# Kernel tuning notes

Hardware: AMD Instinct MI355X
Metric: run time of the kernel (lower is better)

## Reference

```python
import jax, jax.numpy as jnp
import numpy as np

N_AGENTS = 10
N_ENEMIES = 11
N_ALLIES = 9
H = 64           # rnn_hidden_dim
HYP = 64         # api_hyper_dim
DEPTH = 2        # residual_depth
OWN = 32
EF = 10          # enemy_feats_dim
AF = 10          # ally_feats_dim
N_ACTIONS = 17
BS = 1024


def _hypernet(x, win, bin_, wres, bres, wout, bout):
    # Linear -> ReLU -> DEPTH x (ReLU(Linear)+identity) -> Linear
    h = jax.nn.relu(x @ win + bin_)
    for d in range(DEPTH):
        h = jax.nn.relu(h @ wres[d] + bres[d]) + h
    return h @ wout + bout


def _gru_cell(x, h, wi, wh, bi, bh):
    gi = x @ wi + bi
    gh = h @ wh + bh
    ir, iz, in_ = jnp.split(gi, 3, axis=-1)
    hr, hz, hn = jnp.split(gh, 3, axis=-1)
    r = jax.nn.sigmoid(ir + hr)
    z = jax.nn.sigmoid(iz + hz)
    n = jnp.tanh(in_ + r * hn)
    return (1.0 - z) * n + z * h


def setup_inputs() -> dict:
    key = jax.random.key(0)
    ks = iter(jax.random.split(key, 48))
    def p(shape, s=0.1):
        return jax.random.normal(next(ks), shape, jnp.float32) * s
    N = BS * N_AGENTS
    inp = {
        'own_feats':    p((N, OWN), 1.0),
        'enemy_feats':  p((N * N_ENEMIES, EF), 1.0),
        'ally_feats':   p((N * N_ALLIES, AF), 1.0),
        'hidden_state': p((N, H), 1.0),
        'fc1_w': p((OWN, H)), 'fc1_b': p((H,)),
        'agent_emb': p((N_AGENTS, H)), 'action_emb': p((N_ACTIONS, H)),
        'hen_win': p((EF, HYP)), 'hen_bin': p((HYP,)),
        'hen_wres': p((DEPTH, HYP, HYP)), 'hen_bres': p((DEPTH, HYP)),
        'hen_wout': p((HYP, EF * H)), 'hen_bout': p((EF * H,)),
        'hal_win': p((AF, HYP)), 'hal_bin': p((HYP,)),
        'hal_wres': p((DEPTH, HYP, HYP)), 'hal_bres': p((DEPTH, HYP)),
        'hal_wout': p((HYP, AF * H)), 'hal_bout': p((AF * H,)),
        'gru_wi': p((H, 3 * H)), 'gru_wh': p((H, 3 * H)),
        'gru_bi': p((3 * H,)), 'gru_bh': p((3 * H,)),
        'fc2_w': p((H, 6)), 'fc2_b': p((6,)),
        'how_win': p((EF, HYP)), 'how_bin': p((HYP,)),
        'how_wres': p((DEPTH, HYP, HYP)), 'how_bres': p((DEPTH, HYP)),
        'how_wout': p((HYP, H)), 'how_bout': p((H,)),
        'hob_win': p((EF, HYP)), 'hob_bin': p((HYP,)),
        'hob_wres': p((DEPTH, HYP, HYP)), 'hob_bres': p((DEPTH, HYP)),
        'hob_wout': p((HYP, 1)), 'hob_bout': p((1,)),
        'agent_idx': jax.random.randint(next(ks), (N,), 0, N_AGENTS),
        'last_action_idx': jax.random.randint(next(ks), (N,), 0, N_ACTIONS),
        'bs': BS,
    }
    return inp


def reference(own_feats, enemy_feats, ally_feats, hidden_state,
              fc1_w, fc1_b, agent_emb, action_emb,
              hen_win, hen_bin, hen_wres, hen_bres, hen_wout, hen_bout,
              hal_win, hal_bin, hal_wres, hal_bres, hal_wout, hal_bout,
              gru_wi, gru_wh, gru_bi, gru_bh,
              fc2_w, fc2_b,
              how_win, how_bin, how_wres, how_bres, how_wout, how_bout,
              hob_win, hob_bin, hob_wres, hob_bres, hob_wout, hob_bout,
              agent_idx, last_action_idx, bs):
    N = bs * N_AGENTS
    # own embedding + id embeddings
    emb = own_feats @ fc1_w + fc1_b
    emb = emb + agent_emb[agent_idx] + action_emb[last_action_idx]
    # per-enemy hypernet weights [N*NE, EF, H]; bmm + sum-pool over enemies
    w_en = _hypernet(enemy_feats, hen_win, hen_bin, hen_wres, hen_bres,
                     hen_wout, hen_bout).reshape(-1, EF, H)
    emb_en = jnp.einsum('nf,nfh->nh', enemy_feats, w_en)
    emb_en = emb_en.reshape(N, N_ENEMIES, H).sum(axis=1)
    # per-ally hypernet weights + bmm + sum-pool
    w_al = _hypernet(ally_feats, hal_win, hal_bin, hal_wres, hal_bres,
                     hal_wout, hal_bout).reshape(-1, AF, H)
    emb_al = jnp.einsum('nf,nfh->nh', ally_feats, w_al)
    emb_al = emb_al.reshape(N, N_ALLIES, H).sum(axis=1)
    x = jax.nn.relu(emb + emb_en + emb_al)
    hh = _gru_cell(x, hidden_state.reshape(-1, H), gru_wi, gru_wh, gru_bi, gru_bh)
    q_normal = (hh @ fc2_w + fc2_b).reshape(bs, N_AGENTS, 6)
    # attack-action head: hypernet-generated per-enemy weights/biases
    ow = _hypernet(enemy_feats, how_win, how_bin, how_wres, how_bres,
                   how_wout, how_bout).reshape(N, N_ENEMIES, H)
    ob = _hypernet(enemy_feats, hob_win, hob_bin, hob_wres, hob_bres,
                   hob_wout, hob_bout).reshape(N, N_ENEMIES)
    q_attack = (jnp.einsum('nh,neh->ne', hh, ow) + ob).reshape(bs, N_AGENTS, N_ENEMIES)
    q = jnp.concatenate([q_normal, q_attack], axis=-1)
    return q, hh.reshape(bs, N_AGENTS, H)
```

## Files before the change

### kernel.cpp

```cpp
#include <hip/hip_runtime.h>

#define DI static __device__ __forceinline__

typedef short s16x8 __attribute__((ext_vector_type(8)));
typedef float f32x4 __attribute__((ext_vector_type(4)));
typedef float f32x2 __attribute__((ext_vector_type(2)));
typedef unsigned u32x2 __attribute__((ext_vector_type(2)));

DI unsigned short f2b(float f) {
  union { float f; unsigned u; } v; v.f = f;
  return (unsigned short)((v.u + 0x7FFF + ((v.u >> 16) & 1)) >> 16);
}
DI float b2f(unsigned short s) {
  union { unsigned u; float f; } v; v.u = ((unsigned)s) << 16;
  return v.f;
}
DI unsigned cvtpk(float lo, float hi) {
  unsigned r;
  asm("v_cvt_pk_bf16_f32 %0, %1, %2" : "=v"(r) : "v"(lo), "v"(hi));
  return r;
}
DI f32x4 MFMA(s16x8 a, s16x8 b, f32x4 c) {
  return __builtin_amdgcn_mfma_f32_16x16x32_bf16(a, b, c, 0, 0, 0);
}
DI s16x8 ldg8(const unsigned short* p) { return *(const s16x8*)p; }

#define OFF_WEN   0
#define OFF_WAL   10240
#define OFF_WHOW  20480
#define OFF_WHOB  30720
#define OFF_BGEN  40960
#define OFF_BGAL  83968
#define OFF_WIT   126976
#define OFF_WHT   139264
#define OFF_FC1T  151552
#define OFF_FC2E  153600
#define OFF_HOWT  154624
#define OFF_HOBT  158720
#define SH_END    159744
#define B_EMB_EN  (SH_END*2)
#define B_EMB_AL  (B_EMB_EN + 2621440)
#define B_HB      (B_EMB_AL + 2621440)
#define B_GBF     (B_HB + 40960)

#define XSTR 40
#define HSTR 72
#define PSTR 680

__global__ __launch_bounds__(256) void kprep(
    const float* __restrict__ hen_win, const float* __restrict__ hen_wres,
    const float* __restrict__ hal_win, const float* __restrict__ hal_wres,
    const float* __restrict__ how_win, const float* __restrict__ how_wres,
    const float* __restrict__ hob_win, const float* __restrict__ hob_wres,
    const float* __restrict__ hen_wout, const float* __restrict__ hen_bout,
    const float* __restrict__ hal_wout, const float* __restrict__ hal_bout,
    const float* __restrict__ gru_wi, const float* __restrict__ gru_wh,
    const float* __restrict__ fc1_w, const float* __restrict__ fc2_w,
    const float* __restrict__ how_bout, const float* __restrict__ how_wout,
    const float* __restrict__ hob_wout,
    unsigned short* __restrict__ ws)
{
  const int gid = blockIdx.x * 256 + threadIdx.x;
  const int gsz = gridDim.x * 256;
  for (int i = gid; i < 4 * 10240; i += gsz) {
    int s = i / 10240, idx = i - s * 10240;
    const float* win  = (s == 0) ? hen_win  : (s == 1) ? hal_win  : (s == 2) ? how_win  : hob_win;
    const float* wres = (s == 0) ? hen_wres : (s == 1) ? hal_wres : (s == 2) ? how_wres : hob_wres;
    float v;
    if (idx < 2048) { int n = idx >> 5, k = idx & 31; v = (k < 10) ? win[k*64 + n] : 0.f; }
    else { int r = idx - 2048; int d = r >> 12; int r2 = r & 4095; int n = r2 >> 6, k = r2 & 63;
           v = wres[d*4096 + k*64 + n]; }
    ws[s * 10240 + idx] = f2b(v);
  }
  for (int i = gid; i < 2 * 43008; i += gsz) {
    int s = i / 43008, idx = i - s * 43008;
    const float* wout = s ? hal_wout : hen_wout;
    const float* bout = s ? hal_bout : hen_bout;
    int kl = idx & 31, n = (idx >> 5) & 63, c = idx >> 11;
    int kfg = c * 32 + kl;
    float v = 0.f;
    if (kfg < 640)      { int k = kfg / 10, f = kfg - k * 10; v = wout[k*640 + f*64 + n]; }
    else if (kfg < 650) { v = bout[(kfg - 640)*64 + n]; }
    ws[(s ? OFF_BGAL : OFF_BGEN) + idx] = f2b(v);
  }
  for (int i = gid; i < 2 * 12288; i += gsz) {
    int s = i / 12288, idx = i - s * 12288;
    int n = idx >> 6, k = idx & 63;
    const float* w = s ? gru_wh : gru_wi;
    ws[(s ? OFF_WHT : OFF_WIT) + idx] = f2b(w[k*192 + n]);
  }
  for (int i = gid; i < 2048; i += gsz) { int n = i >> 5, k = i & 31; ws[OFF_FC1T + i] = f2b(fc1_w[k*64 + n]); }
  for (int i = gid; i < 1024; i += gsz) {
    int n = i >> 6, k = i & 63;
    float v = 0.f; if (n < 6) v = fc2_w[k*6 + n]; else if (n == 6) v = how_bout[k];
    ws[OFF_FC2E + i] = f2b(v);
  }
  for (int i = gid; i < 4096; i += gsz) ws[OFF_HOWT + i] = f2b(how_wout[i]);
}

template<int TMAX, bool WLAST>
DI void stack_batch(const unsigned short* __restrict__ x_lds,
                    unsigned short* const (&hbp)[TMAX], const int (&tis)[TMAX], int E,
                    const unsigned short* __restrict__ wg,
                    const float* __restrict__ bin, const float* __restrict__ bres,
                    f32x4 (&hval)[TMAX][4])
{
  const int l = threadIdx.x & 63;
  const int lrow = l & 15, gq = l >> 4, lk8 = gq * 8;
  {
    s16x8 wf[4]; f32x4 bv[4];
#pragma unroll
    for (int mt = 0; mt < 4; mt++) {
      wf[mt] = ldg8(wg + (mt*16 + lrow)*32 + lk8);
      bv[mt] = *(const f32x4*)(bin + mt*16 + gq*4);
    }
#pragma unroll
    for (int tt = 0; tt < TMAX; tt++) {
      if (tis[tt] < E) {
        s16x8 xf = *(const s16x8*)&x_lds[(tis[tt]*16 + lrow)*XSTR + lk8];
#pragma unroll
        for (int mt = 0; mt < 4; mt++) {
          f32x4 d = MFMA(wf[mt], xf, f32x4{0.f,0.f,0.f,0.f});
#pragma unroll
          for (int r = 0; r < 4; r++) hval[tt][mt][r] = fmaxf(d[r] + bv[mt][r], 0.f);
        }
        unsigned short* wr = hbp[tt] + lrow*HSTR;
#pragma unroll
        for (int mt = 0; mt < 4; mt++) {
          u32x2 pw;
          pw.x = cvtpk(hval[tt][mt][0], hval[tt][mt][1]);
          pw.y = cvtpk(hval[tt][mt][2], hval[tt][mt][3]);
          *(u32x2*)&wr[mt*16 + gq*4] = pw;
        }
      }
    }
  }
#pragma unroll
  for (int d = 0; d < 2; d++) {
    const unsigned short* wt = wg + 2048 + d * 4096;
    s16x8 wf[4][2]; f32x4 bv[4];
#pragma unroll
    for (int mt = 0; mt < 4; mt++) {
      wf[mt][0] = ldg8(wt + (mt*16 + lrow)*64 + lk8);
      wf[mt][1] = ldg8(wt + (mt*16 + lrow)*64 + 32 + lk8);
      bv[mt] = *(const f32x4*)(bres + d*64 + mt*16 + gq*4);
    }
#pragma unroll
    for (int tt = 0; tt < TMAX; tt++) {
      if (tis[tt] < E) {
        const unsigned short* hr = hbp[tt] + lrow*HSTR;
        s16x8 b0 = *(const s16x8*)&hr[lk8];
        s16x8 b1 = *(const s16x8*)&hr[32 + lk8];
#pragma unroll
        for (int mt = 0; mt < 4; mt++) {
          f32x4 a = MFMA(wf[mt][0], b0, f32x4{0.f,0.f,0.f,0.f});
          a = MFMA(wf[mt][1], b1, a);
#pragma unroll
          for (int r = 0; r < 4; r++)
            hval[tt][mt][r] = fmaxf(a[r] + bv[mt][r], 0.f) + hval[tt][mt][r];
        }
        if (d == 0 || WLAST) {
          unsigned short* wr = hbp[tt] + lrow*HSTR;
#pragma unroll
          for (int mt = 0; mt < 4; mt++) {
            u32x2 pw;
            pw.x = cvtpk(hval[tt][mt][0], hval[tt][mt][1]);
            pw.y = cvtpk(hval[tt][mt][2], hval[tt][mt][3]);
            *(u32x2*)&wr[mt*16 + gq*4] = pw;
          }
        }
      }
    }
  }
}

template<int E>
DI void hyp_body16(const float* __restrict__ feats,
                   const unsigned short* __restrict__ Wg, const unsigned short* __restrict__ Bg,
                   const float* __restrict__ bin, const float* __restrict__ bres,
                   float* __restrict__ emb, char* smem)
{
  unsigned short* x_lds = (unsigned short*)smem;
  unsigned short* h_lds = (unsigned short*)(smem + 14080);
  unsigned short* P     = (unsigned short*)smem;
  const int t = threadIdx.x;
  const int l = t & 63, wv = t >> 6;
  const int lrow = l & 15, gq = l >> 4, lk8 = gq * 8, lr4 = gq * 4;

  for (int idx = t; idx < E * 512; idx += 256) {
    int row = idx >> 5, c = idx & 31;
    x_lds[row*XSTR + c] = (c < 10) ? f2b(feats[row*10 + c]) : (unsigned short)0;
  }
  __syncthreads();

  int tis[3] = {wv, wv + 4, wv + 8};
  unsigned short* hbp[3] = { h_lds + (wv)*16*HSTR, h_lds + (wv+4)*16*HSTR, h_lds + (wv+8)*16*HSTR };
  f32x4 hval[3][4];
  stack_batch<3, true>(x_lds, hbp, tis, E, Wg, bin, bres, hval);
  __syncthreads();

  const int a = t >> 4, kq = t & 15, k0 = kq * 4;
  float acc[4][10];
#pragma unroll
  for (int kk = 0; kk < 4; kk++)
#pragma unroll
    for (int f = 0; f < 10; f++) acc[kk][f] = 0.f;
#pragma unroll
  for (int e = 0; e < E; e++) {
    int row = a * E + e;
    const unsigned short* xr = x_lds + row * XSTR;
    s16x8 xv8 = *(const s16x8*)xr;
    unsigned xv2 = *(const unsigned*)(xr + 8);
    float xf[10];
#pragma unroll
    for (int f = 0; f < 8; f++) xf[f] = b2f((unsigned short)xv8[f]);
    xf[8] = b2f((unsigned short)(xv2 & 0xFFFF));
    xf[9] = b2f((unsigned short)(xv2 >> 16));
    u32x2 hp = *(const u32x2*)&h_lds[row*HSTR + k0];
    float hf[4] = { b2f((unsigned short)(hp.x & 0xFFFF)), b2f((unsigned short)(hp.x >> 16)),
                    b2f((unsigned short)(hp.y & 0xFFFF)), b2f((unsigned short)(hp.y >> 16)) };
#pragma unroll
    for (int kk = 0; kk < 4; kk++)
#pragma unroll
      for (int f = 0; f < 10; f++) acc[kk][f] += hf[kk] * xf[f];
  }
  float sxv = 0.f; int a2 = 0, fx = 0;
  if (t < 160) {
    a2 = t / 10; fx = t - a2 * 10;
    for (int e = 0; e < E; e++) sxv += feats[(a2*E + e)*10 + fx];
  }
  __syncthreads();

  u32x2* Pw = (u32x2*)(P + a*PSTR + k0*10);
#pragma unroll
  for (int m = 0; m < 10; m++) {
    const int s0 = 4*m, s1 = 4*m+1, s2 = 4*m+2, s3 = 4*m+3;
    u32x2 pw;
    pw.x = cvtpk(acc[s0/10][s0%10], acc[s1/10][s1%10]);
    pw.y = cvtpk(acc[s2/10][s2%10], acc[s3/10][s3%10]);
    Pw[m] = pw;
  }
  if (t < 160) P[a2*PSTR + 640 + fx] = f2b(sxv);
  for (int i = t; i < 352; i += 256) { int a3 = i / 22, c = i - a3*22; P[a3*PSTR + 650 + c] = 0; }
  __syncthreads();

  f32x4 acc0 = {0.f,0.f,0.f,0.f}, acc1 = {0.f,0.f,0.f,0.f};
  const unsigned short* Bw = Bg + (wv*16 + lrow)*32 + lk8;
#pragma unroll
  for (int c = 0; c < 21; c++) {
    s16x8 af = *(const s16x8*)&P[lrow*PSTR + c*32 + lk8];
    s16x8 bf = ldg8(Bw + c*2048);
    if (c & 1) acc1 = MFMA(af, bf, acc1); else acc0 = MFMA(af, bf, acc0);
  }
#pragma unroll
  for (int r = 0; r < 4; r++)
    emb[(lr4 + r)*64 + wv*16 + lrow] = acc0[r] + acc1[r];
}

__global__ __launch_bounds__(256) void khyp_ea(
    const float* __restrict__ en_feats, const float* __restrict__ al_feats,
    const unsigned short* __restrict__ ws,
    const float* __restrict__ en_bin, const float* __restrict__ en_bres,
    const float* __restrict__ al_bin, const float* __restrict__ al_bres,
    float* __restrict__ emb_en, float* __restrict__ emb_al)
{
  __shared__ __align__(16) char smem[39424];
  if (blockIdx.x < 640) {
    int blk = blockIdx.x;
    hyp_body16<11>(en_feats + (long)blk*1760, ws + OFF_WEN, ws + OFF_BGEN,
                   en_bin, en_bres, emb_en + (long)blk*1024, smem);
  } else {
    int blk = blockIdx.x - 640;
    hyp_body16<9>(al_feats + (long)blk*1440, ws + OFF_WAL, ws + OFF_BGAL,
                  al_bin, al_bres, emb_al + (long)blk*1024, smem);
  }
}

__global__ __launch_bounds__(256) void kfused(
    const float* __restrict__ own, const float* __restrict__ agent_emb,
    const float* __restrict__ action_emb,
    const int* __restrict__ agent_idx, const int* __restrict__ last_action,
    const float* __restrict__ emb_en, const float* __restrict__ emb_al,
    const float* __restrict__ hidden,
    const unsigned short* __restrict__ ws,
    const float* __restrict__ fc1_b, const float* __restrict__ bi,
    const float* __restrict__ bh, const float* __restrict__ fc2_b,
    float* __restrict__ qout, float* __restrict__ hhout,
    unsigned short* __restrict__ g_bf, float* __restrict__ hb)
{
  __shared__ unsigned short own_lds[16*32];
  __shared__ unsigned short x_lds[16*HSTR];
  __shared__ unsigned short hp_lds[16*HSTR];
  __shared__ unsigned short hh_lds[16*HSTR];
  const int t = threadIdx.x;
  const int l = t & 63, wv = t >> 6;
  const int lrow = l & 15, lk8 = (l >> 4) * 8, lr4 = (l >> 4) * 4;
  const int n0 = blockIdx.x * 16;

  const unsigned short* fc1T = ws + OFF_FC1T;
  const unsigned short* wiT  = ws + OFF_WIT;
  const unsigned short* whT  = ws + OFF_WHT;
  const unsigned short* howT = ws + OFF_HOWT;
  const unsigned short* fc2e = ws + OFF_FC2E;

  for (int i = t; i < 512; i += 256) own_lds[i] = f2b(own[n0*32 + i]);
  for (int i = t; i < 1024; i += 256) hp_lds[(i >> 6)*HSTR + (i & 63)] = f2b(hidden[n0*64 + i]);
  __syncthreads();

  const int j = wv * 16 + lrow;
  {
    s16x8 a0 = *(const s16x8*)&own_lds[lrow*32 + lk8];
    s16x8 b0 = ldg8(fc1T + (wv*16 + lrow)*32 + lk8);
    f32x4 c0 = MFMA(a0, b0, f32x4{0.f,0.f,0.f,0.f});
    float fb = fc1_b[j];
#pragma unroll
    for (int r = 0; r < 4; r++) {
      int aa = lr4 + r; int n = n0 + aa;
      int ai = agent_idx[n], la = last_action[n];
      float v = c0[r] + fb + agent_emb[ai*64 + j] + action_emb[la*64 + j]
              + emb_en[n*64 + j] + emb_al[n*64 + j];
      x_lds[aa*HSTR + j] = f2b(fmaxf(v, 0.f));
    }
  }
  __syncthreads();

  {
    s16x8 xa[2], ha[2];
#pragma unroll
    for (int s = 0; s < 2; s++) {
      xa[s] = *(const s16x8*)&x_lds[lrow*HSTR + s*32 + lk8];
      ha[s] = *(const s16x8*)&hp_lds[lrow*HSTR + s*32 + lk8];
    }
    f32x4 gi[3], gh[3];
#pragma unroll
    for (int g3 = 0; g3 < 3; g3++) { gi[g3] = f32x4{0.f,0.f,0.f,0.f}; gh[g3] = f32x4{0.f,0.f,0.f,0.f}; }
#pragma unroll
    for (int g3 = 0; g3 < 3; g3++) {
      int tl = wv + g3 * 4;
#pragma unroll
      for (int s = 0; s < 2; s++) {
        gi[g3] = MFMA(xa[s], ldg8(wiT + (tl*16 + lrow)*64 + s*32 + lk8), gi[g3]);
        gh[g3] = MFMA(ha[s], ldg8(whT + (tl*16 + lrow)*64 + s*32 + lk8), gh[g3]);
      }
    }
    float bir = bi[j], biz = bi[64 + j], bin_ = bi[128 + j];
    float bhr = bh[j], bhz = bh[64 + j], bhn = bh[128 + j];
#pragma unroll
    for (int r = 0; r < 4; r++) {
      int aa = lr4 + r; int n = n0 + aa;
      float rr = 1.f / (1.f + __expf(-(gi[0][r] + bir + gh[0][r] + bhr)));
      float zz = 1.f / (1.f + __expf(-(gi[1][r] + biz + gh[1][r] + bhz)));
      float nn = tanhf(gi[2][r] + bin_ + rr * (gh[2][r] + bhn));
      float hp = hidden[n*64 + j];
      float hhv = (1.f - zz) * nn + zz * hp;
      hhout[n*64 + j] = hhv;
      hh_lds[aa*HSTR + j] = f2b(hhv);
    }
  }
  __syncthreads();

  {
    s16x8 hha[2];
#pragma unroll
    for (int s = 0; s < 2; s++) hha[s] = *(const s16x8*)&hh_lds[lrow*HSTR + s*32 + lk8];
    f32x4 gc = {0.f,0.f,0.f,0.f};
#pragma unroll
    for (int s = 0; s < 2; s++) gc = MFMA(hha[s], ldg8(howT + (wv*16 + lrow)*64 + s*32 + lk8), gc);
#pragma unroll
    for (int r = 0; r < 4; r++) g_bf[(n0 + lr4 + r)*64 + wv*16 + lrow] = f2b(gc[r]);
    if (wv == 0) {
      f32x4 qc = {0.f,0.f,0.f,0.f};
#pragma unroll
      for (int s = 0; s < 2; s++) qc = MFMA(hha[s], ldg8(fc2e + lrow*64 + s*32 + lk8), qc);
#pragma unroll
      for (int r = 0; r < 4; r++) {
        int n = n0 + lr4 + r;
        if (lrow < 6)       qout[n*17 + lrow] = qc[r] + fc2_b[lrow];
        else if (lrow == 6) hb[n] = qc[r];
      }
    }
  }
}

__global__ __launch_bounds__(256) void kattack(
    const float* __restrict__ en_feats, const unsigned short* __restrict__ ws,
    const float* __restrict__ how_bin, const float* __restrict__ how_bres,
    const float* __restrict__ hob_bin, const float* __restrict__ hob_bres,
    const unsigned short* __restrict__ g_bf, const float* __restrict__ hbuf,
    const float* __restrict__ hob_wout, const float* __restrict__ hob_bout,
    float* __restrict__ qout)
{
  __shared__ __align__(16) char smem[41728];
  unsigned short* x_lds = (unsigned short*)smem;
  unsigned short* scr   = (unsigned short*)(smem + 14080);
  const int t = threadIdx.x;
  const int l = t & 63, wv = t >> 6;
  const int lrow = l & 15, gq = l >> 4;
  const int blk = blockIdx.x;
  const float* feats = en_feats + (long)blk * 1760;

  for (int idx = t; idx < 176*32; idx += 256) {
    int row = idx >> 5, c = idx & 31;
    x_lds[row*XSTR + c] = (c < 10) ? f2b(feats[row*10 + c]) : (unsigned short)0;
  }
  __syncthreads();

  int tis[3] = {wv, wv + 4, wv + 8};
  unsigned short* hbp[3] = { scr + (wv*3+0)*16*HSTR, scr + (wv*3+1)*16*HSTR, scr + (wv*3+2)*16*HSTR };
  f32x4 hval[3][4];

  stack_batch<3, false>(x_lds, hbp, tis, 11, ws + OFF_WHOB, hob_bin, hob_bres, hval);
  f32x4 hw[4];
#pragma unroll
  for (int mt = 0; mt < 4; mt++) hw[mt] = *(const f32x4*)(hob_wout + mt*16 + gq*4);
  float qbv[3] = {0.f, 0.f, 0.f};
#pragma unroll
  for (int tt = 0; tt < 3; tt++) {
    if (tis[tt] < 11) {
      float s = 0.f;
#pragma unroll
      for (int mt = 0; mt < 4; mt++)
#pragma unroll
        for (int r = 0; r < 4; r++) s += hval[tt][mt][r] * hw[mt][r];
      s += __shfl_xor(s, 16, 64);
      s += __shfl_xor(s, 32, 64);
      qbv[tt] = s;
    }
  }

  stack_batch<3, false>(x_lds, hbp, tis, 11, ws + OFF_WHOW, how_bin, how_bres, hval);
  const float hob_b0 = hob_bout[0];
#pragma unroll
  for (int tt = 0; tt < 3; tt++) {
    if (tis[tt] < 11) {
      int row = tis[tt]*16 + lrow;
      int ag = (unsigned)row / 11u;
      int n = blk*16 + ag;
      float s = 0.f;
#pragma unroll
      for (int mt = 0; mt < 4; mt++) {
        u32x2 gv = *(const u32x2*)(g_bf + (long)n*64 + mt*16 + gq*4);
        s += hval[tt][mt][0] * b2f((unsigned short)(gv.x & 0xFFFF))
           + hval[tt][mt][1] * b2f((unsigned short)(gv.x >> 16))
           + hval[tt][mt][2] * b2f((unsigned short)(gv.y & 0xFFFF))
           + hval[tt][mt][3] * b2f((unsigned short)(gv.y >> 16));
      }
      s += __shfl_xor(s, 16, 64);
      s += __shfl_xor(s, 32, 64);
      if (l < 16) {
        int e = row - ag * 11;
        qout[n*17 + 6 + e] = s + qbv[tt] + hbuf[n] + hob_b0;
      }
    }
  }
}

extern "C" void kernel_launch(void* const* d_in, const int* in_sizes, int n_in,
                              void* d_out, int out_size, void* d_ws, size_t ws_size,
                              hipStream_t stream)
{
  (void)in_sizes; (void)n_in; (void)out_size; (void)ws_size;
  const float* own        = (const float*)d_in[0];
  const float* enemy      = (const float*)d_in[1];
  const float* ally       = (const float*)d_in[2];
  const float* hidden     = (const float*)d_in[3];
  const float* fc1_w      = (const float*)d_in[4];
  const float* fc1_b      = (const float*)d_in[5];
  const float* agent_emb  = (const float*)d_in[6];
  const float* action_emb = (const float*)d_in[7];
  const float* hen_win  = (const float*)d_in[8];  const float* hen_bin  = (const float*)d_in[9];
  const float* hen_wres = (const float*)d_in[10]; const float* hen_bres = (const float*)d_in[11];
  const float* hen_wout = (const float*)d_in[12]; const float* hen_bout = (const float*)d_in[13];
  const float* hal_win  = (const float*)d_in[14]; const float* hal_bin  = (const float*)d_in[15];
  const float* hal_wres = (const float*)d_in[16]; const float* hal_bres = (const float*)d_in[17];
  const float* hal_wout = (const float*)d_in[18]; const float* hal_bout = (const float*)d_in[19];
  const float* gru_wi = (const float*)d_in[20];   const float* gru_wh = (const float*)d_in[21];
  const float* gru_bi = (const float*)d_in[22];   const float* gru_bh = (const float*)d_in[23];
  const float* fc2_w  = (const float*)d_in[24];   const float* fc2_b  = (const float*)d_in[25];
  const float* how_win  = (const float*)d_in[26]; const float* how_bin  = (const float*)d_in[27];
  const float* how_wres = (const float*)d_in[28]; const float* how_bres = (const float*)d_in[29];
  const float* how_wout = (const float*)d_in[30]; const float* how_bout = (const float*)d_in[31];
  const float* hob_win  = (const float*)d_in[32]; const float* hob_bin  = (const float*)d_in[33];
  const float* hob_wres = (const float*)d_in[34]; const float* hob_bres = (const float*)d_in[35];
  const float* hob_wout = (const float*)d_in[36]; const float* hob_bout = (const float*)d_in[37];
  const int* agent_idx   = (const int*)d_in[38];
  const int* last_action = (const int*)d_in[39];

  unsigned short* ws = (unsigned short*)d_ws;
  float* emb_en = (float*)((char*)d_ws + B_EMB_EN);
  float* emb_al = (float*)((char*)d_ws + B_EMB_AL);
  float* hb     = (float*)((char*)d_ws + B_HB);
  unsigned short* g_bf = (unsigned short*)((char*)d_ws + B_GBF);

  float* q  = (float*)d_out;
  float* hh = q + 1024*10*17;

  kprep<<<128, 256, 0, stream>>>(hen_win, hen_wres, hal_win, hal_wres,
      how_win, how_wres, hob_win, hob_wres,
      hen_wout, hen_bout, hal_wout, hal_bout,
      gru_wi, gru_wh, fc1_w, fc2_w, how_bout, how_wout, hob_wout, ws);
  khyp_ea<<<1280, 256, 0, stream>>>(enemy, ally, ws,
      hen_bin, hen_bres, hal_bin, hal_bres, emb_en, emb_al);
  kfused<<<640, 256, 0, stream>>>(own, agent_emb, action_emb, agent_idx, last_action,
      emb_en, emb_al, hidden, ws, fc1_b, gru_bi, gru_bh, fc2_b, q, hh, g_bf, hb);
  kattack<<<640, 256, 0, stream>>>(enemy, ws, how_bin, how_bres, hob_bin, hob_bres,
      g_bf, hb, hob_wout, hob_bout, q);
}
```

Measured before the change: 78.49 us.

## Restructure hypernet kernels to one agent per 16-row tile with padded entity planes

The hypernet tiles change from packing 11 or 9 entities contiguously into 16-row MFMA tiles to giving each agent its own 16-row tile, zero-padded to 16 entities, with a compact plane layout in LDS. The per-agent outer product x^T h is now computed with an MFMA instead of scalar FMAs, and blocks handle 8 agents instead of 16, so khyp_ea and kattack launch twice as many blocks with about half the shared memory each. This removes the divergent tile-bound checks and the scalar pooling loop, and should raise occupancy. The cost is wasted MFMA work on padding rows (5/16 or 7/16 of each tile) and more blocks overall.

Result: slower. 106.0 us (+35.0%).

```diff
diff --git a/kernel.cpp b/kernel.cpp
--- a/kernel.cpp
+++ b/kernel.cpp
@@ -4,7 +4,6 @@
 
 typedef short s16x8 __attribute__((ext_vector_type(8)));
 typedef float f32x4 __attribute__((ext_vector_type(4)));
-typedef float f32x2 __attribute__((ext_vector_type(2)));
 typedef unsigned u32x2 __attribute__((ext_vector_type(2)));
 
 DI unsigned short f2b(float f) {
@@ -36,16 +35,14 @@
 #define OFF_FC1T  151552
 #define OFF_FC2E  153600
 #define OFF_HOWT  154624
-#define OFF_HOBT  158720
 #define SH_END    159744
 #define B_EMB_EN  (SH_END*2)
 #define B_EMB_AL  (B_EMB_EN + 2621440)
 #define B_HB      (B_EMB_AL + 2621440)
 #define B_GBF     (B_HB + 40960)
 
-#define XSTR 40
+#define PSTR 680
 #define HSTR 72
-#define PSTR 680
 
 __global__ __launch_bounds__(256) void kprep(
     const float* __restrict__ hen_win, const float* __restrict__ hen_wres,
@@ -57,7 +54,6 @@
     const float* __restrict__ gru_wi, const float* __restrict__ gru_wh,
     const float* __restrict__ fc1_w, const float* __restrict__ fc2_w,
     const float* __restrict__ how_bout, const float* __restrict__ how_wout,
-    const float* __restrict__ hob_wout,
     unsigned short* __restrict__ ws)
 {
   const int gid = blockIdx.x * 256 + threadIdx.x;
@@ -98,14 +94,13 @@
   for (int i = gid; i < 4096; i += gsz) ws[OFF_HOWT + i] = f2b(how_wout[i]);
 }
 
-template<int TMAX, bool WLAST>
-DI void stack_batch(const unsigned short* __restrict__ x_lds,
-                    unsigned short* const (&hbp)[TMAX], const int (&tis)[TMAX], int E,
-                    const unsigned short* __restrict__ wg,
-                    const float* __restrict__ bin, const float* __restrict__ bres,
-                    f32x4 (&hval)[TMAX][4])
-{
-  const int l = threadIdx.x & 63;
+DI void stack_planes(const unsigned short* __restrict__ x_lds,
+                     unsigned short* __restrict__ h2,
+                     const unsigned short* __restrict__ wg,
+                     const float* __restrict__ bin, const float* __restrict__ bres,
+                     f32x4 (&hval)[2][4])
+{
+  const int l = threadIdx.x & 63, wv = threadIdx.x >> 6;
   const int lrow = l & 15, gq = l >> 4, lk8 = gq * 8;
   {
     s16x8 wf[4]; f32x4 bv[4];
@@ -115,146 +110,146 @@
       bv[mt] = *(const f32x4*)(bin + mt*16 + gq*4);
     }
 #pragma unroll
-    for (int tt = 0; tt < TMAX; tt++) {
-      if (tis[tt] < E) {
-        s16x8 xf = *(const s16x8*)&x_lds[(tis[tt]*16 + lrow)*XSTR + lk8];
-#pragma unroll
-        for (int mt = 0; mt < 4; mt++) {
-          f32x4 d = MFMA(wf[mt], xf, f32x4{0.f,0.f,0.f,0.f});
-#pragma unroll
-          for (int r = 0; r < 4; r++) hval[tt][mt][r] = fmaxf(d[r] + bv[mt][r], 0.f);
-        }
-        unsigned short* wr = hbp[tt] + lrow*HSTR;
-#pragma unroll
-        for (int mt = 0; mt < 4; mt++) {
-          u32x2 pw;
-          pw.x = cvtpk(hval[tt][mt][0], hval[tt][mt][1]);
-          pw.y = cvtpk(hval[tt][mt][2], hval[tt][mt][3]);
-          *(u32x2*)&wr[mt*16 + gq*4] = pw;
-        }
+    for (int tt = 0; tt < 2; tt++) {
+      int a = wv + tt*4;
+      s16x8 xf = *(const s16x8*)&x_lds[(a*16 + lrow)*16 + lk8];
+      unsigned short* hw = h2 + a*1024 + lrow*16 + gq*4;
+#pragma unroll
+      for (int mt = 0; mt < 4; mt++) {
+        f32x4 d = MFMA(wf[mt], xf, f32x4{0.f,0.f,0.f,0.f});
+#pragma unroll
+        for (int r = 0; r < 4; r++) hval[tt][mt][r] = fmaxf(d[r] + bv[mt][r], 0.f);
+        u32x2 pw; pw.x = cvtpk(hval[tt][mt][0], hval[tt][mt][1]);
+        pw.y = cvtpk(hval[tt][mt][2], hval[tt][mt][3]);
+        *(u32x2*)(hw + mt*256) = pw;
       }
     }
   }
 #pragma unroll
   for (int d = 0; d < 2; d++) {
     const unsigned short* wt = wg + 2048 + d * 4096;
-    s16x8 wf[4][2]; f32x4 bv[4];
+    s16x8 wf0[4], wf1[4]; f32x4 bv[4];
 #pragma unroll
     for (int mt = 0; mt < 4; mt++) {
-      wf[mt][0] = ldg8(wt + (mt*16 + lrow)*64 + lk8);
-      wf[mt][1] = ldg8(wt + (mt*16 + lrow)*64 + 32 + lk8);
+      wf0[mt] = ldg8(wt + (mt*16 + lrow)*64 + lk8);
+      wf1[mt] = ldg8(wt + (mt*16 + lrow)*64 + 32 + lk8);
       bv[mt] = *(const f32x4*)(bres + d*64 + mt*16 + gq*4);
     }
 #pragma unroll
-    for (int tt = 0; tt < TMAX; tt++) {
-      if (tis[tt] < E) {
-        const unsigned short* hr = hbp[tt] + lrow*HSTR;
-        s16x8 b0 = *(const s16x8*)&hr[lk8];
-        s16x8 b1 = *(const s16x8*)&hr[32 + lk8];
-#pragma unroll
-        for (int mt = 0; mt < 4; mt++) {
-          f32x4 a = MFMA(wf[mt][0], b0, f32x4{0.f,0.f,0.f,0.f});
-          a = MFMA(wf[mt][1], b1, a);
-#pragma unroll
-          for (int r = 0; r < 4; r++)
-            hval[tt][mt][r] = fmaxf(a[r] + bv[mt][r], 0.f) + hval[tt][mt][r];
-        }
-        if (d == 0 || WLAST) {
-          unsigned short* wr = hbp[tt] + lrow*HSTR;
-#pragma unroll
-          for (int mt = 0; mt < 4; mt++) {
-            u32x2 pw;
-            pw.x = cvtpk(hval[tt][mt][0], hval[tt][mt][1]);
-            pw.y = cvtpk(hval[tt][mt][2], hval[tt][mt][3]);
-            *(u32x2*)&wr[mt*16 + gq*4] = pw;
-          }
-        }
-      }
-    }
+    for (int tt = 0; tt < 2; tt++) {
+      int a = wv + tt*4;
+      const unsigned short* hr = h2 + a*1024;
+      s16x8 b0 = *(const s16x8*)&hr[(gq>>1)*256 + lrow*16 + (gq&1)*8];
+      s16x8 b1 = *(const s16x8*)&hr[(2 + (gq>>1))*256 + lrow*16 + (gq&1)*8];
+      unsigned short* hw = h2 + a*1024 + lrow*16 + gq*4;
+#pragma unroll
+      for (int mt = 0; mt < 4; mt++) {
+        f32x4 acc = MFMA(wf0[mt], b0, f32x4{0.f,0.f,0.f,0.f});
+        acc = MFMA(wf1[mt], b1, acc);
+#pragma unroll
+        for (int r = 0; r < 4; r++)
+          hval[tt][mt][r] = fmaxf(acc[r] + bv[mt][r], 0.f) + hval[tt][mt][r];
+        u32x2 pw; pw.x = cvtpk(hval[tt][mt][0], hval[tt][mt][1]);
+        pw.y = cvtpk(hval[tt][mt][2], hval[tt][mt][3]);
+        *(u32x2*)(hw + mt*256) = pw;
+      }
+    }
+  }
+}
+
+DI void stage_x(const float* __restrict__ feats, int E, unsigned short* x_lds) {
+  for (int idx = threadIdx.x; idx < 136*16; idx += 256) {
+    int row = idx >> 4, c = idx & 15;
+    int a = row >> 4, e = row & 15;
+    float v = (a < 8 && e < E && c < 10) ? feats[(a*E + e)*10 + c] : 0.f;
+    x_lds[idx] = f2b(v);
   }
 }
 
 template<int E>
-DI void hyp_body16(const float* __restrict__ feats,
-                   const unsigned short* __restrict__ Wg, const unsigned short* __restrict__ Bg,
-                   const float* __restrict__ bin, const float* __restrict__ bres,
-                   float* __restrict__ emb, char* smem)
+DI void hyp_body(const float* __restrict__ feats,
+                 const unsigned short* __restrict__ Wg, const unsigned short* __restrict__ Bg,
+                 const float* __restrict__ bin, const float* __restrict__ bres,
+                 float* __restrict__ emb, char* smem)
 {
   unsigned short* x_lds = (unsigned short*)smem;
-  unsigned short* h_lds = (unsigned short*)(smem + 14080);
-  unsigned short* P     = (unsigned short*)smem;
+  unsigned short* h2    = (unsigned short*)(smem + 4352);
+  unsigned short* P2    = (unsigned short*)smem;
   const int t = threadIdx.x;
   const int l = t & 63, wv = t >> 6;
-  const int lrow = l & 15, gq = l >> 4, lk8 = gq * 8, lr4 = gq * 4;
-
-  for (int idx = t; idx < E * 512; idx += 256) {
-    int row = idx >> 5, c = idx & 31;
-    x_lds[row*XSTR + c] = (c < 10) ? f2b(feats[row*10 + c]) : (unsigned short)0;
-  }
-  __syncthreads();
-
-  int tis[3] = {wv, wv + 4, wv + 8};
-  unsigned short* hbp[3] = { h_lds + (wv)*16*HSTR, h_lds + (wv+4)*16*HSTR, h_lds + (wv+8)*16*HSTR };
-  f32x4 hval[3][4];
-  stack_batch<3, true>(x_lds, hbp, tis, E, Wg, bin, bres, hval);
-  __syncthreads();
-
-  const int a = t >> 4, kq = t & 15, k0 = kq * 4;
-  float acc[4][10];
-#pragma unroll
-  for (int kk = 0; kk < 4; kk++)
-#pragma unroll
-    for (int f = 0; f < 10; f++) acc[kk][f] = 0.f;
-#pragma unroll
-  for (int e = 0; e < E; e++) {
-    int row = a * E + e;
-    const unsigned short* xr = x_lds + row * XSTR;
-    s16x8 xv8 = *(const s16x8*)xr;
-    unsigned xv2 = *(const unsigned*)(xr + 8);
-    float xf[10];
-#pragma unroll
-    for (int f = 0; f < 8; f++) xf[f] = b2f((unsigned short)xv8[f]);
-    xf[8] = b2f((unsigned short)(xv2 & 0xFFFF));
-    xf[9] = b2f((unsigned short)(xv2 >> 16));
-    u32x2 hp = *(const u32x2*)&h_lds[row*HSTR + k0];
-    float hf[4] = { b2f((unsigned short)(hp.x & 0xFFFF)), b2f((unsigned short)(hp.x >> 16)),
-                    b2f((unsigned short)(hp.y & 0xFFFF)), b2f((unsigned short)(hp.y >> 16)) };
-#pragma unroll
-    for (int kk = 0; kk < 4; kk++)
-#pragma unroll
-      for (int f = 0; f < 10; f++) acc[kk][f] += hf[kk] * xf[f];
-  }
-  float sxv = 0.f; int a2 = 0, fx = 0;
-  if (t < 160) {
-    a2 = t / 10; fx = t - a2 * 10;
-    for (int e = 0; e < E; e++) sxv += feats[(a2*E + e)*10 + fx];
-  }
-  __syncthreads();
-
-  u32x2* Pw = (u32x2*)(P + a*PSTR + k0*10);
-#pragma unroll
-  for (int m = 0; m < 10; m++) {
-    const int s0 = 4*m, s1 = 4*m+1, s2 = 4*m+2, s3 = 4*m+3;
-    u32x2 pw;
-    pw.x = cvtpk(acc[s0/10][s0%10], acc[s1/10][s1%10]);
-    pw.y = cvtpk(acc[s2/10][s2%10], acc[s3/10][s3%10]);
-    Pw[m] = pw;
-  }
-  if (t < 160) P[a2*PSTR + 640 + fx] = f2b(sxv);
-  for (int i = t; i < 352; i += 256) { int a3 = i / 22, c = i - a3*22; P[a3*PSTR + 650 + c] = 0; }
+  const int lrow = l & 15, gq = l >> 4, lk8 = gq * 8;
+
+  stage_x(feats, E, x_lds);
+  __syncthreads();
+
+  f32x4 hval[2][4];
+  stack_planes(x_lds, h2, Wg, bin, bres, hval);
+
+  unsigned pkd[2][4][2];
+#pragma unroll
+  for (int tt = 0; tt < 2; tt++) {
+    int a = wv + tt*4;
+    s16x8 af;
+    if (gq < 2) {
+#pragma unroll
+      for (int j = 0; j < 8; j++) af[j] = (short)x_lds[(a*16 + gq*8 + j)*16 + lrow];
+    } else {
+#pragma unroll
+      for (int j = 0; j < 8; j++) af[j] = 0;
+    }
+#pragma unroll
+    for (int mt = 0; mt < 4; mt++) {
+      s16x8 bf;
+      if (gq < 2) {
+#pragma unroll
+        for (int j = 0; j < 8; j++) bf[j] = (short)h2[a*1024 + mt*256 + (gq*8 + j)*16 + lrow];
+      } else {
+#pragma unroll
+        for (int j = 0; j < 8; j++) bf[j] = 0;
+      }
+      f32x4 p = MFMA(af, bf, f32x4{0.f,0.f,0.f,0.f});
+      pkd[tt][mt][0] = cvtpk(p[0], p[1]);
+      pkd[tt][mt][1] = cvtpk(p[2], p[3]);
+    }
+  }
+  __syncthreads();
+
+#pragma unroll
+  for (int tt = 0; tt < 2; tt++) {
+    int a = wv + tt*4;
+#pragma unroll
+    for (int mt = 0; mt < 4; mt++) {
+      int base = a*PSTR + (mt*16 + lrow)*10 + gq*4;
+      if (gq < 2) {
+        *(unsigned*)&P2[base]     = pkd[tt][mt][0];
+        *(unsigned*)&P2[base + 2] = pkd[tt][mt][1];
+      } else if (gq == 2) {
+        *(unsigned*)&P2[base]     = pkd[tt][mt][0];
+      }
+    }
+  }
+  if (t < 80) {
+    int a = t / 10, fx = t - a*10;
+    float s = 0.f;
+    for (int e = 0; e < E; e++) s += feats[(a*E + e)*10 + fx];
+    P2[a*PSTR + 640 + fx] = f2b(s);
+  }
+  if (t < 176) { int a = t / 22, c = t - (t/22)*22; P2[a*PSTR + 650 + c] = 0; }
   __syncthreads();
 
   f32x4 acc0 = {0.f,0.f,0.f,0.f}, acc1 = {0.f,0.f,0.f,0.f};
   const unsigned short* Bw = Bg + (wv*16 + lrow)*32 + lk8;
 #pragma unroll
   for (int c = 0; c < 21; c++) {
-    s16x8 af = *(const s16x8*)&P[lrow*PSTR + c*32 + lk8];
-    s16x8 bf = ldg8(Bw + c*2048);
-    if (c & 1) acc1 = MFMA(af, bf, acc1); else acc0 = MFMA(af, bf, acc0);
-  }
-#pragma unroll
-  for (int r = 0; r < 4; r++)
-    emb[(lr4 + r)*64 + wv*16 + lrow] = acc0[r] + acc1[r];
+    s16x8 afx = *(const s16x8*)&P2[lrow*PSTR + c*32 + lk8];
+    s16x8 bfx = ldg8(Bw + c*2048);
+    if (c & 1) acc1 = MFMA(afx, bfx, acc1); else acc0 = MFMA(afx, bfx, acc0);
+  }
+  if (gq < 2) {
+#pragma unroll
+    for (int r = 0; r < 4; r++)
+      emb[(gq*4 + r)*64 + wv*16 + lrow] = acc0[r] + acc1[r];
+  }
 }
 
 __global__ __launch_bounds__(256) void khyp_ea(
@@ -264,15 +259,15 @@
     const float* __restrict__ al_bin, const float* __restrict__ al_bres,
     float* __restrict__ emb_en, float* __restrict__ emb_al)
 {
-  __shared__ __align__(16) char smem[39424];
-  if (blockIdx.x < 640) {
+  __shared__ __align__(16) char smem[21760];
+  if (blockIdx.x < 1280) {
     int blk = blockIdx.x;
-    hyp_body16<11>(en_feats + (long)blk*1760, ws + OFF_WEN, ws + OFF_BGEN,
-                   en_bin, en_bres, emb_en + (long)blk*1024, smem);
+    hyp_body<11>(en_feats + (long)blk*880, ws + OFF_WEN, ws + OFF_BGEN,
+                 en_bin, en_bres, emb_en + (long)blk*512, smem);
   } else {
-    int blk = blockIdx.x - 640;
-    hyp_body16<9>(al_feats + (long)blk*1440, ws + OFF_WAL, ws + OFF_BGAL,
-                  al_bin, al_bres, emb_al + (long)blk*1024, smem);
+    int blk = blockIdx.x - 1280;
+    hyp_body<9>(al_feats + (long)blk*720, ws + OFF_WAL, ws + OFF_BGAL,
+                al_bin, al_bres, emb_al + (long)blk*512, smem);
   }
 }
 
@@ -390,68 +385,55 @@
     const float* __restrict__ hob_wout, const float* __restrict__ hob_bout,
     float* __restrict__ qout)
 {
-  __shared__ __align__(16) char smem[41728];
+  __shared__ __align__(16) char smem[20736];
   unsigned short* x_lds = (unsigned short*)smem;
-  unsigned short* scr   = (unsigned short*)(smem + 14080);
+  unsigned short* h2    = (unsigned short*)(smem + 4352);
   const int t = threadIdx.x;
   const int l = t & 63, wv = t >> 6;
   const int lrow = l & 15, gq = l >> 4;
   const int blk = blockIdx.x;
-  const float* feats = en_feats + (long)blk * 1760;
-
-  for (int idx = t; idx < 176*32; idx += 256) {
-    int row = idx >> 5, c = idx & 31;
-    x_lds[row*XSTR + c] = (c < 10) ? f2b(feats[row*10 + c]) : (unsigned short)0;
-  }
-  __syncthreads();
-
-  int tis[3] = {wv, wv + 4, wv + 8};
-  unsigned short* hbp[3] = { scr + (wv*3+0)*16*HSTR, scr + (wv*3+1)*16*HSTR, scr + (wv*3+2)*16*HSTR };
-  f32x4 hval[3][4];
-
-  stack_batch<3, false>(x_lds, hbp, tis, 11, ws + OFF_WHOB, hob_bin, hob_bres, hval);
+  const float* feats = en_feats + (long)blk * 880;
+
+  stage_x(feats, 11, x_lds);
+  __syncthreads();
+
+  f32x4 hval[2][4];
+
+  stack_planes(x_lds, h2, ws + OFF_WHOB, hob_bin, hob_bres, hval);
   f32x4 hw[4];
 #pragma unroll
   for (int mt = 0; mt < 4; mt++) hw[mt] = *(const f32x4*)(hob_wout + mt*16 + gq*4);
-  float qbv[3] = {0.f, 0.f, 0.f};
-#pragma unroll
-  for (int tt = 0; tt < 3; tt++) {
-    if (tis[tt] < 11) {
-      float s = 0.f;
-#pragma unroll
-      for (int mt = 0; mt < 4; mt++)
-#pragma unroll
-        for (int r = 0; r < 4; r++) s += hval[tt][mt][r] * hw[mt][r];
-      s += __shfl_xor(s, 16, 64);
-      s += __shfl_xor(s, 32, 64);
-      qbv[tt] = s;
-    }
-  }
-
-  stack_batch<3, false>(x_lds, hbp, tis, 11, ws + OFF_WHOW, how_bin, how_bres, hval);
+  float qbv[2];
+#pragma unroll
+  for (int tt = 0; tt < 2; tt++) {
+    float s = 0.f;
+#pragma unroll
+    for (int mt = 0; mt < 4; mt++)
+#pragma unroll
+      for (int r = 0; r < 4; r++) s += hval[tt][mt][r] * hw[mt][r];
+    s += __shfl_xor(s, 16, 64);
+    s += __shfl_xor(s, 32, 64);
+    qbv[tt] = s;
+  }
+
+  stack_planes(x_lds, h2, ws + OFF_WHOW, how_bin, how_bres, hval);
   const float hob_b0 = hob_bout[0];
 #pragma unroll
-  for (int tt = 0; tt < 3; tt++) {
-    if (tis[tt] < 11) {
-      int row = tis[tt]*16 + lrow;
-      int ag = (unsigned)row / 11u;
-      int n = blk*16 + ag;
-      float s = 0.f;
-#pragma unroll
-      for (int mt = 0; mt < 4; mt++) {
-        u32x2 gv = *(const u32x2*)(g_bf + (long)n*64 + mt*16 + gq*4);
-        s += hval[tt][mt][0] * b2f((unsigned short)(gv.x & 0xFFFF))
-           + hval[tt][mt][1] * b2f((unsigned short)(gv.x >> 16))
-           + hval[tt][mt][2] * b2f((unsigned short)(gv.y & 0xFFFF))
-           + hval[tt][mt][3] * b2f((unsigned short)(gv.y >> 16));
-      }
-      s += __shfl_xor(s, 16, 64);
-      s += __shfl_xor(s, 32, 64);
-      if (l < 16) {
-        int e = row - ag * 11;
-        qout[n*17 + 6 + e] = s + qbv[tt] + hbuf[n] + hob_b0;
-      }
-    }
+  for (int tt = 0; tt < 2; tt++) {
+    int n = blk*8 + wv + tt*4;
+    float s = 0.f;
+#pragma unroll
+    for (int mt = 0; mt < 4; mt++) {
+      u32x2 gv = *(const u32x2*)(g_bf + (long)n*64 + mt*16 + gq*4);
+      s += hval[tt][mt][0] * b2f((unsigned short)(gv.x & 0xFFFF))
+         + hval[tt][mt][1] * b2f((unsigned short)(gv.x >> 16))
+         + hval[tt][mt][2] * b2f((unsigned short)(gv.y & 0xFFFF))
+         + hval[tt][mt][3] * b2f((unsigned short)(gv.y >> 16));
+    }
+    s += __shfl_xor(s, 16, 64);
+    s += __shfl_xor(s, 32, 64);
+    if (gq == 0 && lrow < 11)
+      qout[n*17 + 6 + lrow] = s + qbv[tt] + hbuf[n] + hob_b0;
   }
 }
 
@@ -498,11 +480,11 @@
   kprep<<<128, 256, 0, stream>>>(hen_win, hen_wres, hal_win, hal_wres,
       how_win, how_wres, hob_win, hob_wres,
       hen_wout, hen_bout, hal_wout, hal_bout,
-      gru_wi, gru_wh, fc1_w, fc2_w, how_bout, how_wout, hob_wout, ws);
-  khyp_ea<<<1280, 256, 0, stream>>>(enemy, ally, ws,
+      gru_wi, gru_wh, fc1_w, fc2_w, how_bout, how_wout, ws);
+  khyp_ea<<<2560, 256, 0, stream>>>(enemy, ally, ws,
       hen_bin, hen_bres, hal_bin, hal_bres, emb_en, emb_al);
   kfused<<<640, 256, 0, stream>>>(own, agent_emb, action_emb, agent_idx, last_action,
       emb_en, emb_al, hidden, ws, fc1_b, gru_bi, gru_bh, fc2_b, q, hh, g_bf, hb);
-  kattack<<<640, 256, 0, stream>>>(enemy, ws, how_bin, how_bres, hob_bin, hob_bres,
+  kattack<<<1280, 256, 0, stream>>>(enemy, ws, how_bin, how_bres, hob_bin, hob_bres,
       g_bf, hb, hob_wout, hob_bout, q);
 }
```
